# Optimization experiments

Hardware: AMD Instinct MI355X
Metric: run time of the kernel (lower is better)

## Reference

```python
import jax, jax.numpy as jnp
import numpy as np

N = 100000          # num_nodes
E = 600000          # num_edges
NUM_EDGE_TYPE = 10
R = 2 * NUM_EDGE_TYPE  # 20 relations (forward + inverse)
DIN, DH, DOUT = 128, 128, 128


def setup_inputs() -> dict:
    key = jax.random.key(0)
    k = jax.random.split(key, 8)
    glorot = lambda kk, shape: jax.random.normal(kk, shape, jnp.float32) * np.sqrt(2.0 / (shape[-2] + shape[-1]))
    return {
        "x": jnp.arange(N, dtype=jnp.int64) if jax.config.jax_enable_x64 else jnp.arange(N, dtype=jnp.int32),
        "edge": jax.random.randint(k[0], (2, E), 0, N),
        "edge_type": jax.random.randint(k[1], (E,), 0, R),
        "emb": jax.random.normal(k[2], (N, DIN), jnp.float32) * 0.02,
        "w1": glorot(k[3], (R, DIN, DH)),
        "root1": glorot(k[4], (DIN, DH)),
        "b1": jnp.zeros((DH,), jnp.float32),
        "w2": glorot(k[5], (R, DH, DOUT)),
        "root2": glorot(k[6], (DH, DOUT)),
        "b2": jnp.zeros((DOUT,), jnp.float32),
    }


def rgcn_conv(h, edge, edge_type, w, root, b):
    # PyG RGCNConv: out = sum_r mean_{j in N_r(i)} W_r x_j + root x_i + b
    src, dst = edge[0], edge[1]
    x_src = h[src]                       # [E, din] gathered source features
    out = h @ root + b                   # root/self transform
    for r in range(R):                   # fixed structural loop over relations
        m = (edge_type == r).astype(h.dtype)                       # [E]
        s = jax.ops.segment_sum(x_src * m[:, None], dst, num_segments=N)  # [N, din]
        c = jax.ops.segment_sum(m, dst, num_segments=N)            # [N] in-degree per relation
        mean = s / jnp.clip(c, 1.0)[:, None]
        out = out + mean @ w[r]          # linear => mean-then-transform == transform-then-mean
    return out


def reference(x, edge, edge_type, emb, w1, root1, b1, w2, root2, b2):
    h = emb[x]                                        # embedding lookup [N, DIN]
    h1 = rgcn_conv(h, edge, edge_type, w1, root1, b1)  # [N, DH]
    h = jax.nn.relu(h1)
    h2 = rgcn_conv(h, edge, edge_type, w2, root2, b2)  # [N, DOUT]
    return h2
```

## Files before the change

### kernel.cpp

```cpp
#include <hip/hip_runtime.h>

#define DD 128
#define RNUM 20

typedef __attribute__((ext_vector_type(4))) float f32x4;
typedef __attribute__((ext_vector_type(8))) short s16x8;
typedef unsigned long long u64;
typedef unsigned int u32;

__device__ inline ushort f2bf(float f) {
    unsigned u = __float_as_uint(f);
    unsigned r = (u + 0x7FFF + ((u >> 16) & 1)) >> 16;
    return (ushort)r;
}

#define M_RCNT 0
#define M_RBASE 20
#define M_RTILE 41
#define M_TOT 88
#define BRSTRIDE 2048


__global__ void k_transpose(const float* w1, const float* root1,
                            const float* w2, const float* root2,
                            ushort* wt1, ushort* wt2) {
    int m = blockIdx.x;
    const float* src;
    ushort* dst;
    if (m < 21) { src = (m == 20) ? root1 : w1 + m * DD * DD; dst = wt1 + m * DD * DD; }
    else { int mm = m - 21; src = (mm == 20) ? root2 : w2 + mm * DD * DD; dst = wt2 + mm * DD * DD; }
    for (int idx = threadIdx.x; idx < DD * DD; idx += blockDim.x) {
        int n = idx >> 7, k = idx & 127;
        dst[idx] = f2bf(src[k * DD + n]);
    }
}

__global__ void k_gather_h(const int* x, const float* emb, ushort* h, int N) {
    int id = blockIdx.x * blockDim.x + threadIdx.x;
    if (id >= N * 32) return;
    int n = id >> 5, c = (id & 31) * 4;
    int xn = x[n];
    float4 v = *(const float4*)(emb + (size_t)xn * DD + c);
    ushort4 o;
    o.x = f2bf(v.x); o.y = f2bf(v.y); o.z = f2bf(v.z); o.w = f2bf(v.w);
    *(ushort4*)(h + (size_t)n * DD + c) = o;
}


__global__ void k_hist(const int* edge, const int* et, int E, u32* cnt) {
    int e = blockIdx.x * 256 + threadIdx.x;
    if (e >= E) return;
    int b = edge[E + e] * RNUM + et[e];
    atomicAdd(&cnt[b], 1u);
}

__global__ __launch_bounds__(256) void k_scan_part(const u32* cnt, int NB, u64* psum, u32* blockrel) {
    __shared__ u64 red[256];
    __shared__ u32 h20[RNUM];
    int t = threadIdx.x;
    if (t < RNUM) h20[t] = 0;
    __syncthreads();
    int base = blockIdx.x * 1024 + t * 4;
    u64 s = 0;
    for (int i = 0; i < 4; i++) {
        int b = base + i;
        if (b < NB) {
            u32 c = cnt[b];
            s += (u64)c | ((u64)(c > 0) << 32);
            if (c) atomicAdd(&h20[b % RNUM], 1u);
        }
    }
    red[t] = s;
    __syncthreads();
    for (int o = 128; o > 0; o >>= 1) {
        if (t < o) red[t] += red[t + o];
        __syncthreads();
    }
    if (t == 0) psum[blockIdx.x] = red[0];
    if (t < RNUM) blockrel[t * BRSTRIDE + blockIdx.x] = h20[t];
}

__global__ __launch_bounds__(256) void k_scan_top(u64* psum, int P, u32* meta,
                                                  u64* escan, int NB, u32* segoff, int N) {
    __shared__ u64 sc[256];
    int t = threadIdx.x;
    u64 loc[8];
    u64 s = 0;
    for (int i = 0; i < 8; i++) {
        int p = t * 8 + i;
        loc[i] = (p < P) ? psum[p] : 0;
        s += loc[i];
    }
    sc[t] = s;
    __syncthreads();
    for (int o = 1; o < 256; o <<= 1) {
        u64 x = (t >= o) ? sc[t - o] : 0;
        __syncthreads();
        sc[t] += x;
        __syncthreads();
    }
    u64 run = sc[t] - s;
    for (int i = 0; i < 8; i++) {
        int p = t * 8 + i;
        if (p < P) { psum[p] = run; run += loc[i]; }
    }
    if (t == 255) {
        u64 tot = sc[255];
        *(u64*)(meta + M_TOT) = tot;
        escan[NB] = tot;
        segoff[N] = (u32)(tot >> 32);
    }
}

__global__ __launch_bounds__(256) void k_scan_add(const u32* cnt, int NB, const u64* psum,
                                                  u64* escan, u32* segoff) {
    __shared__ u64 sc[256];
    int t = threadIdx.x;
    int base = blockIdx.x * 1024 + t * 4;
    u64 v[4];
    u64 s = 0;
    for (int i = 0; i < 4; i++) {
        int b = base + i;
        u32 c = (b < NB) ? cnt[b] : 0;
        v[i] = (u64)c | ((u64)(c > 0) << 32);
        s += v[i];
    }
    sc[t] = s;
    __syncthreads();
    for (int o = 1; o < 256; o <<= 1) {
        u64 x = (t >= o) ? sc[t - o] : 0;
        __syncthreads();
        sc[t] += x;
        __syncthreads();
    }
    u64 run = psum[blockIdx.x] + sc[t] - s;
    for (int i = 0; i < 4; i++) {
        int b = base + i;
        if (b < NB) {
            escan[b] = run;
            if (b % RNUM == 0) segoff[b / RNUM] = (u32)(run >> 32);
            run += v[i];
        }
    }
}

__global__ __launch_bounds__(256) void k_colscan2(u32* blockrel, int P, u32* meta) {
    __shared__ u32 sc[256];
    int c = blockIdx.x;
    int t = threadIdx.x;
    u32* col = blockrel + c * BRSTRIDE;
    u32 v[8];
    u32 s = 0;
#pragma unroll
    for (int i = 0; i < 8; i++) {
        int p = t * 8 + i;
        v[i] = (p < P) ? col[p] : 0;
        s += v[i];
    }
    sc[t] = s;
    __syncthreads();
    for (int o = 1; o < 256; o <<= 1) {
        u32 x = (t >= o) ? sc[t - o] : 0;
        __syncthreads();
        sc[t] += x;
        __syncthreads();
    }
    u32 run = sc[t] - s;
#pragma unroll
    for (int i = 0; i < 8; i++) {
        int p = t * 8 + i;
        if (p < P) { col[p] = run; run += v[i]; }
    }
    if (t == 255) meta[M_RCNT + c] = sc[255];
}

__global__ void k_rscan(u32* meta) {
    if (threadIdx.x || blockIdx.x) return;
    u32 off = 0, toff = 0;
    for (int r = 0; r < RNUM; r++) {
        meta[M_RBASE + r] = off;
        meta[M_RTILE + r] = toff;
        u32 c = meta[M_RCNT + r];
        off += c;
        toff += (c + 63) >> 6;
    }
    meta[M_RBASE + RNUM] = off;
    meta[M_RTILE + RNUM] = toff;
}

__global__ __launch_bounds__(256) void k_build(const u32* cnt, const u64* escan, int NB,
                                               const u32* __restrict__ meta,
                                               const u32* __restrict__ blockrel,
                                               u32* segmeta, u32* rseg) {
    __shared__ u32 h20[RNUM];
    int t = threadIdx.x;
    if (t < RNUM) h20[t] = 0;
    __syncthreads();
    int base = blockIdx.x * 1024 + t * 4;
    for (int i = 0; i < 4; i++) {
        int b = base + i;
        if (b >= NB) break;
        u32 c = cnt[b];
        if (!c) continue;
        int r = b % RNUM;
        u32 my = atomicAdd(&h20[r], 1u);
        u64 e = escan[b];
        u32 s = (u32)(e >> 32);
        segmeta[s] = ((u32)e & 0xFFFFFu) | (c << 20);
        rseg[meta[M_RBASE + r] + blockrel[r * BRSTRIDE + blockIdx.x] + my] = s;
    }
}

__global__ void k_scatter2(const int* edge, const int* et, int E,
                           const u64* escan, u32* cnt, int* bsrc2) {
    int e = blockIdx.x * 256 + threadIdx.x;
    if (e >= E) return;
    int b = edge[E + e] * RNUM + et[e];
    u32 old = atomicSub(&cnt[b], 1u);
    u32 pos = (u32)escan[b] + old - 1;
    bsrc2[pos] = edge[e];
}


__global__ __launch_bounds__(256, 4) void k_agg_gemm(const ushort* __restrict__ h,
                                                     const ushort* __restrict__ wt,
                                                     const int* __restrict__ bsrc2,
                                                     const u32* __restrict__ segmeta,
                                                     const u32* __restrict__ rseg,
                                                     const u32* __restrict__ meta,
                                                     ushort* __restrict__ Y) {
    __shared__ __align__(16) char Al[64 * 256];
    __shared__ int ssid[64];
    int tile = blockIdx.x;
    if (tile >= (int)meta[M_RTILE + RNUM]) return;
    int r = 0;
#pragma unroll
    for (int i = 1; i < RNUM; i++)
        if (tile >= (int)meta[M_RTILE + i]) r = i;
    int j0 = (tile - (int)meta[M_RTILE + r]) * 64;
    int nseg = (int)meta[M_RCNT + r];
    u32 rb = meta[M_RBASE + r];
    int t = threadIdx.x;
    int j = t >> 2, t4 = t & 3;
    {
        char* arow = Al + j * 256;
        int swz = (j & 7) << 4;
        int sj = j0 + j;
        int s = -1;
        int c = 0, epos = 0;
        if (sj < nseg) {
            s = (int)rseg[rb + sj];
            u32 m = segmeta[s];
            epos = m & 0xFFFFF;
            c = (int)(m >> 20);
        }
        if (t4 == 0) ssid[j] = s;
        if (c == 1) {
            int src = bsrc2[epos];
            const ushort* hp = h + (size_t)src * DD + t4 * 32;
#pragma unroll
            for (int k = 0; k < 4; k++) {
                s16x8 v = *(const s16x8*)(hp + k * 8);
                *(s16x8*)(arow + ((t4 * 64 + k * 16) ^ swz)) = v;
            }
        } else {
            float a[32];
#pragma unroll
            for (int i = 0; i < 32; i++) a[i] = 0.f;
            for (int q = 0; q < c; q++) {
                int src = bsrc2[epos + q];
                const ushort* hp = h + (size_t)src * DD + t4 * 32;
#pragma unroll
                for (int k = 0; k < 4; k++) {
                    s16x8 v = *(const s16x8*)(hp + k * 8);
#pragma unroll
                    for (int i = 0; i < 8; i++)
                        a[k * 8 + i] += __uint_as_float(((u32)(ushort)v[i]) << 16);
                }
            }
            float inv = (c > 0) ? (1.0f / (float)c) : 0.f;
#pragma unroll
            for (int i = 0; i < 32; i++) a[i] *= inv;
#pragma unroll
            for (int k = 0; k < 4; k++) {
                s16x8 o;
#pragma unroll
                for (int i = 0; i < 8; i++) o[i] = (short)f2bf(a[k * 8 + i]);
                *(s16x8*)(arow + ((t4 * 64 + k * 16) ^ swz)) = o;
            }
        }
    }
    int w = t >> 6, l = t & 63, lr = l & 15, lg = l >> 4;
    const ushort* wr = wt + (size_t)r * DD * DD;
    s16x8 bq[2][4];
#pragma unroll
    for (int cc = 0; cc < 2; cc++)
#pragma unroll
        for (int ks = 0; ks < 4; ks++)
            bq[cc][ks] = *(const s16x8*)(wr + (size_t)(w * 32 + cc * 16 + lr) * DD + ks * 32 + lg * 8);
    __syncthreads();
    f32x4 acc[4][2];
#pragma unroll
    for (int rt = 0; rt < 4; rt++)
#pragma unroll
        for (int cc = 0; cc < 2; cc++) acc[rt][cc] = (f32x4){0.f, 0.f, 0.f, 0.f};
#pragma unroll
    for (int ks = 0; ks < 4; ks++) {
#pragma unroll
        for (int rt = 0; rt < 4; rt++) {
            s16x8 af = *(const s16x8*)(Al + (rt * 16 + lr) * 256 + ((ks * 64 + lg * 16) ^ ((lr & 7) << 4)));
#pragma unroll
            for (int cc = 0; cc < 2; cc++)
                acc[rt][cc] = __builtin_amdgcn_mfma_f32_16x16x32_bf16(af, bq[cc][ks], acc[rt][cc], 0, 0, 0);
        }
    }
#pragma unroll
    for (int rt = 0; rt < 4; rt++) {
#pragma unroll
        for (int q = 0; q < 4; q++) {
            int row = rt * 16 + lg * 4 + q;
            int s = ssid[row];
            if (s < 0) continue;
            ushort* yp = Y + (size_t)s * DD + w * 32;
#pragma unroll
            for (int cc = 0; cc < 2; cc++)
                yp[cc * 16 + lr] = f2bf(acc[rt][cc][q]);
        }
    }
}

template <int RELU>
__global__ __launch_bounds__(256, 4) void k_out(const ushort* __restrict__ h,
                                                const ushort* __restrict__ wroot,
                                                const float* __restrict__ bias,
                                                const ushort* __restrict__ Y,
                                                const u32* __restrict__ segoff,
                                                ushort* __restrict__ hout,
                                                float* __restrict__ fout, int N) {
    __shared__ __align__(16) char U[64 * 132 * 4];
    float* Cl = (float*)U;
    __shared__ float biasl[DD];
    int n0 = blockIdx.x * 64;
    int t = threadIdx.x;
    if (t < DD) biasl[t] = bias[t];
    for (int q = t; q < 1024; q += 256) {
        int row = q >> 4, cb = q & 15;
        int i = n0 + row;
        int4 v = make_int4(0, 0, 0, 0);
        if (i < N) v = *(const int4*)(h + (size_t)i * DD + cb * 8);
        *(int4*)(U + row * 256 + ((cb * 16) ^ ((row & 7) << 4))) = v;
    }
    int w = t >> 6, l = t & 63, lr = l & 15, lg = l >> 4;
    s16x8 bq[2][4];
#pragma unroll
    for (int cc = 0; cc < 2; cc++)
#pragma unroll
        for (int ks = 0; ks < 4; ks++)
            bq[cc][ks] = *(const s16x8*)(wroot + (size_t)(w * 32 + cc * 16 + lr) * DD + ks * 32 + lg * 8);
    __syncthreads();
    f32x4 acc[4][2];
#pragma unroll
    for (int rt = 0; rt < 4; rt++)
#pragma unroll
        for (int cc = 0; cc < 2; cc++) acc[rt][cc] = (f32x4){0.f, 0.f, 0.f, 0.f};
#pragma unroll
    for (int ks = 0; ks < 4; ks++) {
#pragma unroll
        for (int rt = 0; rt < 4; rt++) {
            s16x8 af = *(const s16x8*)(U + (rt * 16 + lr) * 256 + ((ks * 64 + lg * 16) ^ ((lr & 7) << 4)));
#pragma unroll
            for (int cc = 0; cc < 2; cc++)
                acc[rt][cc] = __builtin_amdgcn_mfma_f32_16x16x32_bf16(af, bq[cc][ks], acc[rt][cc], 0, 0, 0);
        }
    }
    __syncthreads();
#pragma unroll
    for (int rt = 0; rt < 4; rt++) {
#pragma unroll
        for (int q = 0; q < 4; q++) {
            int row = rt * 16 + lg * 4 + q;
#pragma unroll
            for (int cc = 0; cc < 2; cc++)
                Cl[row * 132 + w * 32 + cc * 16 + lr] = acc[rt][cc][q];
        }
    }
    __syncthreads();
    int j = t >> 2, t4 = t & 3;
    int node = n0 + j;
    if (node >= N) return;
    float a[32];
#pragma unroll
    for (int k = 0; k < 8; k++) {
        f32x4 cv = *(const f32x4*)(Cl + j * 132 + t4 * 32 + k * 4);
        a[k * 4 + 0] = cv[0]; a[k * 4 + 1] = cv[1]; a[k * 4 + 2] = cv[2]; a[k * 4 + 3] = cv[3];
    }
    u32 s0 = segoff[node], s1 = segoff[node + 1];
    for (u32 s = s0; s < s1; s++) {
        const ushort* yp = Y + (size_t)s * DD + t4 * 32;
#pragma unroll
        for (int k = 0; k < 4; k++) {
            s16x8 v = *(const s16x8*)(yp + k * 8);
#pragma unroll
            for (int i = 0; i < 8; i++)
                a[k * 8 + i] += __uint_as_float(((u32)(ushort)v[i]) << 16);
        }
    }
#pragma unroll
    for (int i = 0; i < 32; i++) a[i] += biasl[t4 * 32 + i];
    if (RELU) {
        ushort* op = hout + (size_t)node * DD + t4 * 32;
#pragma unroll
        for (int k = 0; k < 4; k++) {
            s16x8 o;
#pragma unroll
            for (int i = 0; i < 8; i++) {
                float xv = a[k * 8 + i];
                o[i] = (short)f2bf(xv > 0.f ? xv : 0.f);
            }
            *(s16x8*)(op + k * 8) = o;
        }
    } else {
#pragma unroll
        for (int k = 0; k < 8; k++) {
            f32x4 o = (f32x4){a[k * 4 + 0], a[k * 4 + 1], a[k * 4 + 2], a[k * 4 + 3]};
            *(f32x4*)(fout + (size_t)node * DD + t4 * 32 + k * 4) = o;
        }
    }
}


extern "C" void kernel_launch(void* const* d_in, const int* in_sizes, int n_in,
                              void* d_out, int out_size, void* d_ws, size_t ws_size,
                              hipStream_t stream) {
    const int* x = (const int*)d_in[0];
    const int* edge = (const int*)d_in[1];
    const int* etype = (const int*)d_in[2];
    const float* emb = (const float*)d_in[3];
    const float* w1 = (const float*)d_in[4];
    const float* root1 = (const float*)d_in[5];
    const float* b1 = (const float*)d_in[6];
    const float* w2 = (const float*)d_in[7];
    const float* root2 = (const float*)d_in[8];
    const float* b2 = (const float*)d_in[9];
    float* out = (float*)d_out;

    const int N = in_sizes[0];
    const int E = in_sizes[2];
    const int NB = N * RNUM;

    char* p = (char*)d_ws;
    auto alloc = [&](size_t bytes) {
        char* q = p;
        p += (bytes + 255) & ~(size_t)255;
        return q;
    };
    int* bsrc2 = (int*)alloc((size_t)E * 4);
    u32* segmeta = (u32*)alloc((size_t)E * 4);
    u32* rseg = (u32*)alloc((size_t)E * 4);
    u32* segoff = (u32*)alloc((size_t)(N + 1) * 4);
    u32* meta = (u32*)alloc(512);
    u32* blockrel = (u32*)alloc((size_t)RNUM * BRSTRIDE * 4);
    ushort* wt1 = (ushort*)alloc((size_t)21 * DD * DD * 2);
    ushort* wt2 = (ushort*)alloc((size_t)21 * DD * DD * 2);
    ushort* hbuf = (ushort*)alloc((size_t)N * DD * 2);
    u64* escan = (u64*)alloc((size_t)(NB + 1) * 8);
    u32* cnt = (u32*)alloc((size_t)NB * 4);
    u64* psum = (u64*)alloc(2048 * 8);
    ushort* Y = (ushort*)escan;
    {
        char* yend = (char*)escan + (size_t)E * DD * 2;
        if (yend > p) p = yend;
    }

    hipMemsetAsync(cnt, 0, (size_t)NB * 4, stream);
    hipMemsetAsync(meta, 0, 512, stream);

    int blkE = (E + 255) / 256;
    int blkH = (N * 32 + 255) / 256;
    int P = (NB + 1023) / 1024;
    int TILES = (E + 63) / 64 + RNUM;
    int blkOut = (N + 63) / 64;

    k_transpose<<<42, 256, 0, stream>>>(w1, root1, w2, root2, wt1, wt2);
    k_gather_h<<<blkH, 256, 0, stream>>>(x, emb, hbuf, N);
    k_hist<<<blkE, 256, 0, stream>>>(edge, etype, E, cnt);
    k_scan_part<<<P, 256, 0, stream>>>(cnt, NB, psum, blockrel);
    k_scan_top<<<1, 256, 0, stream>>>(psum, P, meta, escan, NB, segoff, N);
    k_scan_add<<<P, 256, 0, stream>>>(cnt, NB, psum, escan, segoff);
    k_colscan2<<<RNUM, 256, 0, stream>>>(blockrel, P, meta);
    k_rscan<<<1, 64, 0, stream>>>(meta);
    k_build<<<P, 256, 0, stream>>>(cnt, escan, NB, meta, blockrel, segmeta, rseg);
    k_scatter2<<<blkE, 256, 0, stream>>>(edge, etype, E, escan, cnt, bsrc2);

    k_agg_gemm<<<TILES, 256, 0, stream>>>(hbuf, wt1, bsrc2, segmeta, rseg, meta, Y);
    k_out<1><<<blkOut, 256, 0, stream>>>(hbuf, wt1 + 20 * DD * DD, b1, Y, segoff, hbuf, nullptr, N);

    k_agg_gemm<<<TILES, 256, 0, stream>>>(hbuf, wt2, bsrc2, segmeta, rseg, meta, Y);
    k_out<0><<<blkOut, 256, 0, stream>>>(hbuf, wt2 + 20 * DD * DD, b2, Y, segoff, nullptr, out, N);
}
```

Measured before the change: 466.8 us.

## Fuse embedding gather with histogram, raise occupancy, use bf16 LDS staging in k_out

```diff
diff --git a/kernel.cpp b/kernel.cpp
--- a/kernel.cpp
+++ b/kernel.cpp
@@ -35,24 +35,23 @@
     }
 }
 
-__global__ void k_gather_h(const int* x, const float* emb, ushort* h, int N) {
-    int id = blockIdx.x * blockDim.x + threadIdx.x;
-    if (id >= N * 32) return;
-    int n = id >> 5, c = (id & 31) * 4;
-    int xn = x[n];
-    float4 v = *(const float4*)(emb + (size_t)xn * DD + c);
-    ushort4 o;
-    o.x = f2bf(v.x); o.y = f2bf(v.y); o.z = f2bf(v.z); o.w = f2bf(v.w);
-    *(ushort4*)(h + (size_t)n * DD + c) = o;
-}
-
-
-__global__ void k_hist(const int* edge, const int* et, int E, u32* cnt) {
-    int e = blockIdx.x * 256 + threadIdx.x;
-    if (e >= E) return;
-    int b = edge[E + e] * RNUM + et[e];
-    atomicAdd(&cnt[b], 1u);
-}
+__global__ void k_pre(const int* x, const float* emb, ushort* h, int N,
+                      const int* edge, const int* et, int E, u32* cnt) {
+    int id = blockIdx.x * 256 + threadIdx.x;
+    if (id < N * 32) {
+        int n = id >> 5, c = (id & 31) * 4;
+        int xn = x[n];
+        float4 v = *(const float4*)(emb + (size_t)xn * DD + c);
+        ushort4 o;
+        o.x = f2bf(v.x); o.y = f2bf(v.y); o.z = f2bf(v.z); o.w = f2bf(v.w);
+        *(ushort4*)(h + (size_t)n * DD + c) = o;
+    }
+    if (id < E) {
+        int b = edge[E + id] * RNUM + et[id];
+        atomicAdd(&cnt[b], 1u);
+    }
+}
+
 
 __global__ __launch_bounds__(256) void k_scan_part(const u32* cnt, int NB, u64* psum, u32* blockrel) {
     __shared__ u64 red[256];
@@ -222,7 +221,7 @@
 }
 
 
-__global__ __launch_bounds__(256, 4) void k_agg_gemm(const ushort* __restrict__ h,
+__global__ __launch_bounds__(256, 8) void k_agg_gemm(const ushort* __restrict__ h,
                                                      const ushort* __restrict__ wt,
                                                      const int* __restrict__ bsrc2,
                                                      const u32* __restrict__ segmeta,
@@ -330,15 +329,15 @@
 }
 
 template <int RELU>
-__global__ __launch_bounds__(256, 4) void k_out(const ushort* __restrict__ h,
+__global__ __launch_bounds__(256, 6) void k_out(const ushort* __restrict__ h,
                                                 const ushort* __restrict__ wroot,
                                                 const float* __restrict__ bias,
                                                 const ushort* __restrict__ Y,
                                                 const u32* __restrict__ segoff,
                                                 ushort* __restrict__ hout,
                                                 float* __restrict__ fout, int N) {
-    __shared__ __align__(16) char U[64 * 132 * 4];
-    float* Cl = (float*)U;
+    __shared__ __align__(16) char U[64 * 272];
+    ushort* Clb = (ushort*)U;
     __shared__ float biasl[DD];
     int n0 = blockIdx.x * 64;
     int t = threadIdx.x;
@@ -381,7 +380,7 @@
             int row = rt * 16 + lg * 4 + q;
 #pragma unroll
             for (int cc = 0; cc < 2; cc++)
-                Cl[row * 132 + w * 32 + cc * 16 + lr] = acc[rt][cc][q];
+                Clb[row * 136 + w * 32 + cc * 16 + lr] = f2bf(acc[rt][cc][q]);
         }
     }
     __syncthreads();
@@ -390,9 +389,11 @@
     if (node >= N) return;
     float a[32];
 #pragma unroll
-    for (int k = 0; k < 8; k++) {
-        f32x4 cv = *(const f32x4*)(Cl + j * 132 + t4 * 32 + k * 4);
-        a[k * 4 + 0] = cv[0]; a[k * 4 + 1] = cv[1]; a[k * 4 + 2] = cv[2]; a[k * 4 + 3] = cv[3];
+    for (int k = 0; k < 4; k++) {
+        s16x8 cv = *(const s16x8*)(Clb + j * 136 + t4 * 32 + k * 8);
+#pragma unroll
+        for (int i = 0; i < 8; i++)
+            a[k * 8 + i] = __uint_as_float(((u32)(ushort)cv[i]) << 16);
     }
     u32 s0 = segoff[node], s1 = segoff[node + 1];
     for (u32 s = s0; s < s1; s++) {
@@ -477,13 +478,13 @@
 
     int blkE = (E + 255) / 256;
     int blkH = (N * 32 + 255) / 256;
+    int blkPre = blkH > blkE ? blkH : blkE;
     int P = (NB + 1023) / 1024;
     int TILES = (E + 63) / 64 + RNUM;
     int blkOut = (N + 63) / 64;
 
     k_transpose<<<42, 256, 0, stream>>>(w1, root1, w2, root2, wt1, wt2);
-    k_gather_h<<<blkH, 256, 0, stream>>>(x, emb, hbuf, N);
-    k_hist<<<blkE, 256, 0, stream>>>(edge, etype, E, cnt);
+    k_pre<<<blkPre, 256, 0, stream>>>(x, emb, hbuf, N, edge, etype, E, cnt);
     k_scan_part<<<P, 256, 0, stream>>>(cnt, NB, psum, blockrel);
     k_scan_top<<<1, 256, 0, stream>>>(psum, P, meta, escan, NB, segoff, N);
     k_scan_add<<<P, 256, 0, stream>>>(cnt, NB, psum, escan, segoff);
```

After: 481.9 us. 3.2% more time.
